# Kernel tuning notes

Hardware: AMD Instinct MI355X
Metric: run time of the kernel (lower is better)

Reference implementation:

```python
import jax, jax.numpy as jnp
import numpy as np

# regular 3x3 kernel grid: row0 = dy (i-1), row1 = dx (j-1), k = 3*i + j
RY = jnp.array([-1., -1., -1., 0., 0., 0., 1., 1., 1.], dtype=jnp.float32)
RX = jnp.array([-1., 0., 1., -1., 0., 1., -1., 0., 1.], dtype=jnp.float32)


def conv2d(x, w, b):
    # 3x3, stride 1, pad 1, NCHW/OIHW
    out = jax.lax.conv_general_dilated(
        x, w, window_strides=(1, 1), padding=((1, 1), (1, 1)),
        dimension_numbers=('NCHW', 'OIHW', 'NCHW'))
    return out + b[None, :, None, None]


def group_norm(x, gamma, beta, num_groups, eps=1e-5):
    N, C, H, W = x.shape
    xg = x.reshape(N, num_groups, C // num_groups, H, W)
    mu = xg.mean(axis=(2, 3, 4), keepdims=True)
    var = xg.var(axis=(2, 3, 4), keepdims=True)
    xn = ((xg - mu) * jax.lax.rsqrt(var + eps)).reshape(N, C, H, W)
    return xn * gamma[None, :, None, None] + beta[None, :, None, None]


def build_offset(tm, tr):
    # tm: [N,4,H,W] per-pixel 2x2 affine [[m00,m01],[m10,m11]]; tr: [N,2,H,W] (ty, tx)
    m00, m01, m10, m11 = tm[:, 0], tm[:, 1], tm[:, 2], tm[:, 3]  # [N,H,W]
    ry = RY[None, :, None, None]
    rx = RX[None, :, None, None]
    # offset = M @ R - R, plus translation broadcast to all 9 points
    dy = m00[:, None] * ry + m01[:, None] * rx - ry + tr[:, 0:1]  # [N,9,H,W]
    dx = m10[:, None] * ry + m11[:, None] * rx - rx + tr[:, 1:2]  # [N,9,H,W]
    return dy, dx


def bilinear_sample(img, py, px):
    # img: [N,C,H,W]; py, px: [N,K,H,W] sampling locations; zero padding outside
    N, C, H, W = img.shape
    K = py.shape[1]
    y0f = jnp.floor(py)
    x0f = jnp.floor(px)
    wy1 = py - y0f
    wx1 = px - x0f
    wy0 = 1.0 - wy1
    wx0 = 1.0 - wx1
    y0 = y0f.astype(jnp.int32)
    x0 = x0f.astype(jnp.int32)
    img_flat = img.reshape(N, C, H * W)

    def gather(yi, xi):
        valid = ((yi >= 0) & (yi < H) & (xi >= 0) & (xi < W)).astype(img.dtype)
        idx = jnp.clip(yi, 0, H - 1) * W + jnp.clip(xi, 0, W - 1)  # [N,K,H,W]
        flat = idx.reshape(N, 1, K * H * W)
        vals = jnp.take_along_axis(img_flat, jnp.broadcast_to(flat, (N, C, K * H * W)), axis=2)
        return vals.reshape(N, C, K, H, W) * valid[:, None]

    v00 = gather(y0, x0)
    v01 = gather(y0, x0 + 1)
    v10 = gather(y0 + 1, x0)
    v11 = gather(y0 + 1, x0 + 1)
    return (v00 * (wy0 * wx0)[:, None] + v01 * (wy0 * wx1)[:, None]
            + v10 * (wy1 * wx0)[:, None] + v11 * (wy1 * wx1)[:, None])


def deform_conv(x, dy, dx, w, pad=1, dil=1):
    # x: [N,Cin,H,W]; dy,dx: [N,9,H,W]; w: [Cout,Cin,3,3]; stride 1
    N, C, H, W = x.shape
    k = jnp.arange(9)
    ki = (k // 3).astype(x.dtype)[None, :, None, None]
    kj = (k % 3).astype(x.dtype)[None, :, None, None]
    hh = jnp.arange(H, dtype=x.dtype)[None, None, :, None]
    ww = jnp.arange(W, dtype=x.dtype)[None, None, None, :]
    py = hh - pad + dil * ki + dy  # [N,9,H,W]
    px = ww - pad + dil * kj + dx
    sampled = bilinear_sample(x, py, px)  # [N,C,9,H,W]
    return jnp.einsum('nckhw,ock->nohw', sampled, w.reshape(w.shape[0], C, 9))


def setup_inputs() -> dict:
    key = jax.random.key(0)
    ks = jax.random.split(key, 16)
    N, C, H, W = 4, 256, 64, 64
    x = jax.random.normal(ks[0], (N, C, H, W), jnp.float32)
    def p(k, shape, s):
        return jax.random.normal(k, shape, jnp.float32) * s
    s_off = 0.01                       # small STN heads -> modest offsets
    s_dc = 1.0 / np.sqrt(C * 9.0)      # deform-conv fan-in init
    return {
        'x': x,
        'w_tm1': p(ks[1], (4, C, 3, 3), s_off), 'b_tm1': jnp.zeros((4,), jnp.float32),
        'w_tr1': p(ks[2], (2, C, 3, 3), s_off), 'b_tr1': jnp.zeros((2,), jnp.float32),
        'w_dc1': p(ks[3], (C, C, 3, 3), s_dc),
        'g1': jnp.ones((C,), jnp.float32), 'be1': jnp.zeros((C,), jnp.float32),
        'w_tm2': p(ks[4], (4, C, 3, 3), s_off), 'b_tm2': jnp.zeros((4,), jnp.float32),
        'w_tr2': p(ks[5], (2, C, 3, 3), s_off), 'b_tr2': jnp.zeros((2,), jnp.float32),
        'w_dc2': p(ks[6], (C, C, 3, 3), s_dc),
        'g2': jnp.ones((C,), jnp.float32), 'be2': jnp.zeros((C,), jnp.float32),
    }


def reference(x, w_tm1, b_tm1, w_tr1, b_tr1, w_dc1, g1, be1,
              w_tm2, b_tm2, w_tr2, b_tr2, w_dc2, g2, be2):
    GROUPS = 32
    residual = x
    dy1, dx1 = build_offset(conv2d(x, w_tm1, b_tm1), conv2d(x, w_tr1, b_tr1))
    out = deform_conv(x, dy1, dx1, w_dc1)
    out = jax.nn.relu(group_norm(out, g1, be1, GROUPS))
    dy2, dx2 = build_offset(conv2d(out, w_tm2, b_tm2), conv2d(out, w_tr2, b_tr2))
    out = deform_conv(out, dy2, dx2, w_dc2)
    out = group_norm(out, g2, be2, GROUPS)
    return jax.nn.relu(out + residual)
```

## Files before the change

### kernel.cpp

```cpp
#include <hip/hip_runtime.h>


typedef unsigned int u32;
typedef unsigned short u16;
typedef __attribute__((ext_vector_type(8))) short bf16x8;
typedef __attribute__((ext_vector_type(4))) float floatx4;

#define HW 4096
#define CHW 1048576

static __device__ __forceinline__ float bf2f(u16 u) {
    union { u32 i; float f; } c; c.i = ((u32)u) << 16; return c.f;
}
static __device__ __forceinline__ u16 f2bf(float f) {
    union { float f; u32 i; } c; c.f = f;
    u32 x = c.i;
    return (u16)((x + 0x7FFFu + ((x >> 16) & 1u)) >> 16);
}
static __device__ __forceinline__ u32 cvtpk(float a, float b) {
    u32 r;
    asm("v_cvt_pk_bf16_f32 %0, %1, %2" : "=v"(r) : "v"(a), "v"(b));
    return r;
}
static __device__ __forceinline__ void lbar() {
    __builtin_amdgcn_sched_barrier(0);
    asm volatile("s_waitcnt lgkmcnt(0)" ::: "memory");
    __builtin_amdgcn_s_barrier();
    __builtin_amdgcn_sched_barrier(0);
}
static __device__ __forceinline__ float loadv(const void* p, long i, int f32) {
    return f32 ? ((const float*)p)[i] : bf2f(((const u16*)p)[i]);
}
static __device__ __forceinline__ int sniff_f32(const u32* __restrict__ xw) {
    int cnt = 0;
    #pragma unroll
    for (int s = 0; s < 16; ++s) {
        union { u32 i; float f; } c;
        c.i = xw[s * 131 + 7];
        float a = fabsf(c.f);
        if (a > 1e-8f && a < 1e4f) ++cnt;
    }
    return (cnt >= 8) ? 1 : 0;
}

__global__ __launch_bounds__(256) void k_prep_all(
    const void* __restrict__ x,
    const void* __restrict__ wdc1, const void* __restrict__ wdc2,
    const void* __restrict__ wtm1, const void* __restrict__ wtr1,
    const void* __restrict__ wtm2, const void* __restrict__ wtr2,
    u16* __restrict__ xT, u16* __restrict__ wTg1, u16* __restrict__ wTg2,
    u16* __restrict__ wT61, u16* __restrict__ wT62)
{
    __shared__ u16 T[32 * 258];
    const int f32 = sniff_f32((const u32*)x);
    const int b = blockIdx.x;
    const int tid = threadIdx.x;

    if (b < 512) {
        const int n = b >> 7, h = (b >> 1) & 63, half = b & 1;
        const int wbase = half << 5;
        const long sb = (long)n * CHW + (h << 6) + wbase;
        const int cb = tid >> 3;
        const int w0 = (tid & 7) << 2;
        if (f32) {
            const float* xp = (const float*)x;
            for (int it = 0; it < 8; ++it) {
                int c = (it << 5) + cb;
                float4 a = *(const float4*)(xp + sb + (long)c * HW + w0);
                T[(w0 + 0) * 258 + c] = f2bf(a.x);
                T[(w0 + 1) * 258 + c] = f2bf(a.y);
                T[(w0 + 2) * 258 + c] = f2bf(a.z);
                T[(w0 + 3) * 258 + c] = f2bf(a.w);
            }
        } else {
            const u16* xp = (const u16*)x;
            for (int it = 0; it < 8; ++it) {
                int c = (it << 5) + cb;
                uint2 v = *(const uint2*)(xp + sb + (long)c * HW + w0);
                T[(w0 + 0) * 258 + c] = (u16)(v.x & 0xFFFFu);
                T[(w0 + 1) * 258 + c] = (u16)(v.x >> 16);
                T[(w0 + 2) * 258 + c] = (u16)(v.y & 0xFFFFu);
                T[(w0 + 3) * 258 + c] = (u16)(v.y >> 16);
            }
        }
        __syncthreads();
        const int w = tid >> 3, cq = tid & 7;
        const u32* Tr = (const u32*)T;
        u16* ob = xT + (long)n * CHW + (long)((h << 6) + wbase + w) * 256 + cq * 32;
        #pragma unroll
        for (int s = 0; s < 4; ++s) {
            uint4 o;
            o.x = Tr[129 * w + 16 * cq + 4 * s + 0];
            o.y = Tr[129 * w + 16 * cq + 4 * s + 1];
            o.z = Tr[129 * w + 16 * cq + 4 * s + 2];
            o.w = Tr[129 * w + 16 * cq + 4 * s + 3];
            *(uint4*)&ob[s * 8] = o;
        }
    } else if (b < 2816) {
        const int r2 = (b >= 1664);
        const void* wdc = r2 ? wdc2 : wdc1;
        u16* wTg = r2 ? wTg2 : wTg1;
        int idx2 = (b - (r2 ? 1664 : 512)) * 256 + tid;
        int cp = idx2 & 15;
        int o  = (idx2 >> 4) & 255;
        int q  = idx2 >> 12;
        int k  = q >> 3;
        int c0 = ((q & 7) << 5) + (cp << 1);
        long s0 = (long)o * 2304 + c0 * 9 + k;
        ((u32*)wTg)[idx2] = cvtpk(loadv(wdc, s0, f32), loadv(wdc, s0 + 9, f32));
    } else {
        const int r2 = (b >= 2960);
        const void* wtm = r2 ? wtm2 : wtm1;
        const void* wtr = r2 ? wtr2 : wtr1;
        u16* wT6 = r2 ? wT62 : wT61;
        int i = (b - (r2 ? 2960 : 2816)) * 256 + tid;
        int q  = i >> 9;
        int o  = (i >> 5) & 15;
        int cc = i & 31;
        int k  = q >> 3;
        int c  = ((q & 7) << 5) + cc;
        float v = 0.f;
        if (o < 4)      v = loadv(wtm, (long)o * 2304 + c * 9 + k, f32);
        else if (o < 6) v = loadv(wtr, (long)(o - 4) * 2304 + c * 9 + k, f32);
        wT6[i] = f2bf(v);
    }
}

__global__ __launch_bounds__(1024, 4) void k_deform(
    const u16* __restrict__ srcT, const u16* __restrict__ wTg,
    const u16* __restrict__ wT6,
    const void* __restrict__ b_tm, const void* __restrict__ b_tr,
    const u32* __restrict__ xw,
    u16* __restrict__ raw, float* __restrict__ pstats, const int nhwc)
{
    __shared__ __align__(16) char shm[65536];
    __shared__ float tl[6 * 64];
    __shared__ int   g_y0[576];
    __shared__ int   g_x0[576];
    __shared__ float g_wy[576];
    __shared__ float g_wx[576];

    const int tid = threadIdx.x;
    const int bid = blockIdx.x;
    const int n = bid >> 6, h = bid & 63;
    const int lane = tid & 63;
    const int quad = lane >> 4;
    const int l16  = lane & 15;
    const int wv   = tid >> 6;
    const long nbase = (long)n * CHW;
    const u16* sp = srcT + nbase;

    {
        float (*red)[64][17] = (float (*)[64][17])shm;
        if (wv < 8) {
            floatx4 acc6[4];
            #pragma unroll
            for (int j = 0; j < 4; ++j) acc6[j] = (floatx4){0.f, 0.f, 0.f, 0.f};
            for (int qi = 0; qi < 9; ++qi) {
                const int q = wv * 9 + qi;
                const int k = q >> 3, cb = q & 7;
                const int ky = k / 3, kx = k % 3;
                const int row = h + ky - 1;
                const bool rv = (row >= 0) && (row < 64);
                bf16x8 av = *(const bf16x8*)&wT6[(((q << 4) + l16) << 5) + (quad << 3)];
                #pragma unroll
                for (int j = 0; j < 4; ++j) {
                    int psrc = (j << 4) + l16 + kx - 1;
                    bf16x8 bv = {0, 0, 0, 0, 0, 0, 0, 0};
                    if (rv && psrc >= 0 && psrc < 64)
                        bv = *(const bf16x8*)&sp[(((long)(row << 6) + psrc) << 8) + (cb << 5) + (quad << 3)];
                    acc6[j] = __builtin_amdgcn_mfma_f32_16x16x32_bf16(av, bv, acc6[j], 0, 0, 0);
                }
            }
            #pragma unroll
            for (int j = 0; j < 4; ++j)
                #pragma unroll
                for (int r = 0; r < 4; ++r)
                    red[wv][(j << 4) + l16][(quad << 2) + r] = acc6[j][r];
        }
        __syncthreads();
        if (tid < 384) {
            const int o = tid >> 6, px = tid & 63;
            float s = 0.f;
            #pragma unroll
            for (int v = 0; v < 8; ++v) s += red[v][px][o];
            const int f32 = sniff_f32(xw);
            float bias = (o < 4) ? loadv(b_tm, o, f32) : loadv(b_tr, o - 4, f32);
            tl[o * 64 + px] = s + bias;
        }
        __syncthreads();
    }

    if (tid < 576) {
        int i = tid;
        int k = i >> 6, ww2 = i & 63;
        float m00 = tl[ww2],        m01 = tl[64 + ww2];
        float m10 = tl[128 + ww2],  m11 = tl[192 + ww2];
        float tr0 = tl[256 + ww2],  tr1 = tl[320 + ww2];
        float ry = (float)(k / 3) - 1.f;
        float rx = (float)(k % 3) - 1.f;
        float dy = m00 * ry + m01 * rx - ry + tr0;
        float dx = m10 * ry + m11 * rx - rx + tr1;
        float py = (float)h + ry + dy;
        float px = (float)ww2 + rx + dx;
        float y0f = floorf(py), x0f = floorf(px);
        g_y0[i] = (int)y0f; g_x0[i] = (int)x0f;
        g_wy[i] = py - y0f; g_wx[i] = px - x0f;
    }
    __syncthreads();

    const int px   = tid >> 4;
    const int slot = tid & 15;
    const int kh   = wv >> 3;
    const int o0   = (wv & 7) << 5;
    const u32 xw_s = (u32)((px  & 7) << 2);
    const u32 xsw  = (u32)((l16 & 7) << 2);
    const u32 q4x  = (u32)(quad << 2);
    const u32 kh64 = (u32)(kh << 6);

    u32* Sl = (u32*)shm;

    floatx4 acc[2][4];
    #pragma unroll
    for (int a = 0; a < 2; ++a)
        #pragma unroll
        for (int g = 0; g < 4; ++g) acc[a][g] = (floatx4){0.f, 0.f, 0.f, 0.f};

    const int wlane = ((o0 + l16) << 5) + (quad << 3);
    const u16* wk = wTg + (kh << 15);

    u32 o00, o01, o10, o11;
    float cw00, cw01, cw10, cw11;
    const char* spb = (const char*)sp + (slot << 4);

    auto mkptr = [&](int k) {
        int gi = (k << 6) + px;
        int y0 = g_y0[gi], x0 = g_x0[gi];
        int yc0 = min(max(y0, 0), 63),     yc1 = min(max(y0 + 1, 0), 63);
        int xc0 = min(max(x0, 0), 63),     xc1 = min(max(x0 + 1, 0), 63);
        o00 = (u32)(((yc0 << 6) + xc0) << 9);
        o01 = (u32)(((yc0 << 6) + xc1) << 9);
        o10 = (u32)(((yc1 << 6) + xc0) << 9);
        o11 = (u32)(((yc1 << 6) + xc1) << 9);
    };
    auto mkcw = [&](int k) {
        int gi = (k << 6) + px;
        int y0 = g_y0[gi], x0 = g_x0[gi];
        float wy1 = g_wy[gi], wx1 = g_wx[gi];
        float wy0 = 1.f - wy1, wx0 = 1.f - wx1;
        bool yv0 = (y0 >= 0) && (y0 < 64);
        bool yv1 = (y0 >= -1) && (y0 < 63);
        bool xv0 = (x0 >= 0) && (x0 < 64);
        bool xv1 = (x0 >= -1) && (x0 < 63);
        cw00 = (yv0 && xv0) ? wy0 * wx0 : 0.f;
        cw01 = (yv0 && xv1) ? wy0 * wx1 : 0.f;
        cw10 = (yv1 && xv0) ? wy1 * wx0 : 0.f;
        cw11 = (yv1 && xv1) ? wy1 * wx1 : 0.f;
    };

    uint4 GA, GB, GC, GD, HA, HB, HC, HD;
    auto GATHER = [&]() {
        GA = *(const uint4*)(spb + o00);  HA = *(const uint4*)(spb + o00 + 256);
        GB = *(const uint4*)(spb + o01);  HB = *(const uint4*)(spb + o01 + 256);
        GC = *(const uint4*)(spb + o10);  HC = *(const uint4*)(spb + o10 + 256);
        GD = *(const uint4*)(spb + o11);  HD = *(const uint4*)(spb + o11 + 256);
    };

    bf16x8 W0[4], W1[4];

#define BIL(a, b, c, d) cvtpk( \
    fmaf(cw00, bf2f((u16)(a)), fmaf(cw01, bf2f((u16)(b)), \
    fmaf(cw10, bf2f((u16)(c)), cw11 * bf2f((u16)(d))))), \
    fmaf(cw00, bf2f((u16)((a) >> 16)), fmaf(cw01, bf2f((u16)((b) >> 16)), \
    fmaf(cw10, bf2f((u16)((c) >> 16)), cw11 * bf2f((u16)((d) >> 16))))))

    mkptr(0); GATHER();
    W0[0] = *(const bf16x8*)(wk + wlane);
    W1[0] = *(const bf16x8*)(wk + wlane + 512);
    W0[1] = *(const bf16x8*)(wk + 8192 + wlane);
    W1[1] = *(const bf16x8*)(wk + 8192 + wlane + 512);

    for (int k = 0; k < 9; ++k) {
        const int buf = k & 1;
        mkcw(k);
        uint4 v0 = make_uint4(BIL(GA.x, GB.x, GC.x, GD.x), BIL(GA.y, GB.y, GC.y, GD.y),
                              BIL(GA.z, GB.z, GC.z, GD.z), BIL(GA.w, GB.w, GC.w, GD.w));
        uint4 v1 = make_uint4(BIL(HA.x, HB.x, HC.x, HD.x), BIL(HA.y, HB.y, HC.y, HD.y),
                              BIL(HA.z, HB.z, HC.z, HD.z), BIL(HA.w, HB.w, HC.w, HD.w));
        u32* wp = &Sl[((u32)(buf << 13)) + ((u32)(px << 7)) + (((u32)(slot << 2)) ^ xw_s)];
        *(uint4*)wp = v0;
        *(uint4*)(wp + 64) = v1;
        if (k < 8) { mkptr(k + 1); GATHER(); }
        lbar();
        const u32* sb = &Sl[(u32)(buf << 13)];
        #pragma unroll
        for (int c = 0; c < 4; ++c) {
            const u32 offc = (((kh64 + (u32)(c << 4))) | q4x) ^ xsw;
            bf16x8 b0 = *(const bf16x8*)(sb + ((u32)(( 0 + l16) << 7)) + offc);
            bf16x8 b1 = *(const bf16x8*)(sb + ((u32)((16 + l16) << 7)) + offc);
            bf16x8 b2 = *(const bf16x8*)(sb + ((u32)((32 + l16) << 7)) + offc);
            bf16x8 b3 = *(const bf16x8*)(sb + ((u32)((48 + l16) << 7)) + offc);
            if (k < 8 || c < 2) {
                const int tc = c + 2;
                const u16* wb = wk + ((tc & 3) + ((tc >> 2) << 3)) * 8192;
                W0[tc & 3] = *(const bf16x8*)(wb + wlane);
                W1[tc & 3] = *(const bf16x8*)(wb + wlane + 512);
            }
            acc[0][0] = __builtin_amdgcn_mfma_f32_16x16x32_bf16(W0[c], b0, acc[0][0], 0, 0, 0);
            acc[0][1] = __builtin_amdgcn_mfma_f32_16x16x32_bf16(W0[c], b1, acc[0][1], 0, 0, 0);
            acc[0][2] = __builtin_amdgcn_mfma_f32_16x16x32_bf16(W0[c], b2, acc[0][2], 0, 0, 0);
            acc[0][3] = __builtin_amdgcn_mfma_f32_16x16x32_bf16(W0[c], b3, acc[0][3], 0, 0, 0);
            acc[1][0] = __builtin_amdgcn_mfma_f32_16x16x32_bf16(W1[c], b0, acc[1][0], 0, 0, 0);
            acc[1][1] = __builtin_amdgcn_mfma_f32_16x16x32_bf16(W1[c], b1, acc[1][1], 0, 0, 0);
            acc[1][2] = __builtin_amdgcn_mfma_f32_16x16x32_bf16(W1[c], b2, acc[1][2], 0, 0, 0);
            acc[1][3] = __builtin_amdgcn_mfma_f32_16x16x32_bf16(W1[c], b3, acc[1][3], 0, 0, 0);
        }
        wk += 65536;
    }
#undef BIL

    __syncthreads();
    {
        float* ms = (float*)shm;
        if (kh == 1) {
            #pragma unroll
            for (int a = 0; a < 2; ++a)
                #pragma unroll
                for (int g = 0; g < 4; ++g)
                    *(floatx4*)&ms[((((wv & 7) << 3) + (a << 2) + g) << 8) + (lane << 2)] = acc[a][g];
        }
        __syncthreads();
        if (kh == 0) {
            #pragma unroll
            for (int a = 0; a < 2; ++a)
                #pragma unroll
                for (int g = 0; g < 4; ++g) {
                    floatx4 t = *(const floatx4*)&ms[((((wv & 7) << 3) + (a << 2) + g) << 8) + (lane << 2)];
                    acc[a][g] += t;
                }
        }
    }

    if (kh == 0) {
        #pragma unroll
        for (int a = 0; a < 2; ++a) {
            float s1 = 0.f, s2 = 0.f;
            #pragma unroll
            for (int g = 0; g < 4; ++g)
                #pragma unroll
                for (int r = 0; r < 4; ++r) {
                    float v = acc[a][g][r];
                    s1 += v; s2 += v * v;
                }
            #pragma unroll
            for (int off = 1; off <= 16; off <<= 1) {
                s1 += __shfl_xor(s1, off, 64);
                s2 += __shfl_xor(s2, off, 64);
            }
            if ((lane & 31) == 0) {
                int gg = (o0 >> 3) + (a << 1) + (lane >> 5);
                pstats[((long)bid << 6) + (gg << 1)]     = s1;
                pstats[((long)bid << 6) + (gg << 1) + 1] = s2;
            }
        }

        if (nhwc) {
            u16* rb = raw + nbase + ((long)h << 14);
            #pragma unroll
            for (int a = 0; a < 2; ++a)
                #pragma unroll
                for (int g = 0; g < 4; ++g) {
                    int pxe = (g << 4) + l16;
                    int o = o0 + (a << 4) + (quad << 2);
                    u32 lo = cvtpk(acc[a][g][0], acc[a][g][1]);
                    u32 hi = cvtpk(acc[a][g][2], acc[a][g][3]);
                    *(uint2*)&rb[(pxe << 8) + o] = make_uint2(lo, hi);
                }
        } else {
            #pragma unroll
            for (int a = 0; a < 2; ++a)
                #pragma unroll
                for (int g = 0; g < 4; ++g)
                    #pragma unroll
                    for (int r = 0; r < 4; ++r) {
                        int o = o0 + (a << 4) + (quad << 2) + r;
                        raw[nbase + ((long)o << 12) + (h << 6) + (g << 4) + l16]
                            = f2bf(acc[a][g][r]);
                    }
        }
    }
}

__global__ __launch_bounds__(256) void k_gn_relu(
    const u16* __restrict__ raw, const float* __restrict__ pstats,
    const void* __restrict__ gamma, const void* __restrict__ beta,
    const u32* __restrict__ xw,
    u16* __restrict__ out1)
{
    __shared__ float sred[4][64];
    __shared__ float sl[64];
    const int f32 = sniff_f32(xw);
    const int tid = threadIdx.x;
    const int bid = blockIdx.x;
    const int n = bid >> 9;

    {
        const int v = tid & 63, part = tid >> 6;
        float a = 0.f;
        for (int j = part * 16; j < part * 16 + 16; ++j)
            a += pstats[(((long)n * 64 + j) << 6) + v];
        sred[part][v] = a;
        __syncthreads();
        if (tid < 64) sl[tid] = sred[0][tid] + sred[1][tid] + sred[2][tid] + sred[3][tid];
        __syncthreads();
    }

    const long i = (((long)bid) << 8) + tid;
    const int c0 = (int)((i << 3) & 255);
    const int g = c0 >> 3;
    float mean = sl[g * 2] * (1.f / 32768.f);
    float var  = sl[g * 2 + 1] * (1.f / 32768.f) - mean * mean;
    float rstd = rsqrtf(var + 1e-5f);

    float ga[8], be[8];
    if (f32) {
        float4 a0 = ((const float4*)gamma)[c0 >> 2];
        float4 a1 = ((const float4*)gamma)[(c0 >> 2) + 1];
        float4 b0 = ((const float4*)beta)[c0 >> 2];
        float4 b1 = ((const float4*)beta)[(c0 >> 2) + 1];
        ga[0]=a0.x; ga[1]=a0.y; ga[2]=a0.z; ga[3]=a0.w;
        ga[4]=a1.x; ga[5]=a1.y; ga[6]=a1.z; ga[7]=a1.w;
        be[0]=b0.x; be[1]=b0.y; be[2]=b0.z; be[3]=b0.w;
        be[4]=b1.x; be[5]=b1.y; be[6]=b1.z; be[7]=b1.w;
    } else {
        uint4 av = ((const uint4*)gamma)[c0 >> 3];
        uint4 bv = ((const uint4*)beta)[c0 >> 3];
        u32 aw[4] = {av.x, av.y, av.z, av.w};
        u32 bw[4] = {bv.x, bv.y, bv.z, bv.w};
        #pragma unroll
        for (int q = 0; q < 4; ++q) {
            ga[2*q] = bf2f((u16)(aw[q] & 0xFFFFu)); ga[2*q+1] = bf2f((u16)(aw[q] >> 16));
            be[2*q] = bf2f((u16)(bw[q] & 0xFFFFu)); be[2*q+1] = bf2f((u16)(bw[q] >> 16));
        }
    }

    uint4 p = ((const uint4*)raw)[i];
    u32 ww[4] = {p.x, p.y, p.z, p.w};
    u32 o[4];
    #pragma unroll
    for (int q = 0; q < 4; ++q) {
        float g0 = ga[2*q] * rstd,     g1 = ga[2*q+1] * rstd;
        float b0 = be[2*q] - mean*g0,  b1 = be[2*q+1] - mean*g1;
        float a = fmaxf(fmaf(bf2f((u16)(ww[q] & 0xFFFFu)), g0, b0), 0.f);
        float b = fmaxf(fmaf(bf2f((u16)(ww[q] >> 16)),     g1, b1), 0.f);
        o[q] = cvtpk(a, b);
    }
    ((uint4*)out1)[i] = make_uint4(o[0], o[1], o[2], o[3]);
}

__global__ __launch_bounds__(256) void k_gn_final(
    const u16* __restrict__ raw, const float* __restrict__ pstats,
    const void* __restrict__ gamma, const void* __restrict__ beta,
    const void* __restrict__ x,
    void* __restrict__ outp)
{
    __shared__ float rr[256];
    const int f32 = sniff_f32((const u32*)x);
    const int tid = threadIdx.x;
    const long e0 = ((long)blockIdx.x) << 11;
    const int n = (int)(e0 >> 20);
    const int c0 = (int)((e0 >> 12) & 255);
    const int g = c0 >> 3;

    {
        int j = tid & 127, sv = tid >> 7;
        rr[tid] = (j < 64) ? pstats[(((long)n * 64 + j) << 6) + (g << 1) + sv] : 0.f;
        __syncthreads();
        #pragma unroll
        for (int s = 64; s >= 1; s >>= 1) {
            if ((tid & 127) < s) rr[tid] += rr[tid + s];
            __syncthreads();
        }
    }
    float mean = rr[0] * (1.f / 32768.f);
    float var  = rr[128] * (1.f / 32768.f) - mean * mean;
    float rstd = rsqrtf(var + 1e-5f);

    const long i = blockIdx.x * 256 + tid;
    const long e = i << 3;
    const int c = (int)((e >> 12) & 255);
    float ga = loadv(gamma, c, f32) * rstd;
    float be = loadv(beta, c, f32) - mean * ga;
    uint4 p = ((const uint4*)raw)[i];
    u32 ww[4] = {p.x, p.y, p.z, p.w};
    float v[8];
    #pragma unroll
    for (int q = 0; q < 4; ++q) {
        v[2 * q + 0] = fmaxf(fmaf(bf2f((u16)(ww[q] & 0xFFFFu)), ga, be) + loadv(x, e + 2 * q + 0, f32), 0.f);
        v[2 * q + 1] = fmaxf(fmaf(bf2f((u16)(ww[q] >> 16)),     ga, be) + loadv(x, e + 2 * q + 1, f32), 0.f);
    }
    if (f32) {
        float4* op = (float4*)((float*)outp + e);
        op[0] = make_float4(v[0], v[1], v[2], v[3]);
        op[1] = make_float4(v[4], v[5], v[6], v[7]);
    } else {
        uint4 o;
        o.x = cvtpk(v[0], v[1]);
        o.y = cvtpk(v[2], v[3]);
        o.z = cvtpk(v[4], v[5]);
        o.w = cvtpk(v[6], v[7]);
        ((uint4*)outp)[i] = o;
    }
}

extern "C" void kernel_launch(void* const* d_in, const int* in_sizes, int n_in,
                              void* d_out, int out_size, void* d_ws, size_t ws_size,
                              hipStream_t stream) {
    const void* x     = d_in[0];
    const void* w_tm1 = d_in[1];
    const void* b_tm1 = d_in[2];
    const void* w_tr1 = d_in[3];
    const void* b_tr1 = d_in[4];
    const void* w_dc1 = d_in[5];
    const void* g1    = d_in[6];
    const void* be1   = d_in[7];
    const void* w_tm2 = d_in[8];
    const void* b_tm2 = d_in[9];
    const void* w_tr2 = d_in[10];
    const void* b_tr2 = d_in[11];
    const void* w_dc2 = d_in[12];
    const void* g2    = d_in[13];
    const void* be2   = d_in[14];

    char* wsb = (char*)d_ws;
    u16*   xT     = (u16*)wsb;
    u16*   raw    = (u16*)(wsb + 8388608);
    u16*   wTg1   = (u16*)(wsb + 16777216);
    u16*   wTg2   = (u16*)(wsb + 17956864);
    u16*   wT61   = (u16*)(wsb + 19136512);
    u16*   wT62   = (u16*)(wsb + 19210240);
    float* pstats = (float*)(wsb + 19283968);
    u16*   out1   = xT;
    const u32* xw = (const u32*)x;

    k_prep_all<<<3104, 256, 0, stream>>>(x, w_dc1, w_dc2, w_tm1, w_tr1, w_tm2, w_tr2,
                                         xT, wTg1, wTg2, wT61, wT62);
    k_deform  <<<256, 1024, 0, stream>>>(xT, wTg1, wT61, b_tm1, b_tr1, xw, raw, pstats, 1);
    k_gn_relu <<<2048, 256, 0, stream>>>(raw, pstats, g1, be1, xw, out1);
    k_deform  <<<256, 1024, 0, stream>>>(out1, wTg2, wT62, b_tm2, b_tr2, xw, raw, pstats, 0);
    k_gn_final<<<2048, 256, 0, stream>>>(raw, pstats, g2, be2, x, d_out);
}
```

Baseline: 211.6 us.

## Fuse group-norm epilogues into deform kernels via cooperative grid sync

The deform conv kernel becomes a cooperative kernel. After writing per-block partial statistics it does a grid-wide sync, reduces the group statistics in shared memory, and applies GroupNorm+ReLU (or GroupNorm+residual+ReLU) straight from the accumulator registers. This removes the bf16 raw intermediate round trip through global memory and two separate elementwise kernel launches. In exchange, all blocks must be co-resident and wait at a grid barrier, and the final-mode stores stay scalar and strided per channel.

```diff
diff --git a/kernel.cpp b/kernel.cpp
--- a/kernel.cpp
+++ b/kernel.cpp
@@ -1,4 +1,7 @@
 #include <hip/hip_runtime.h>
+#include <hip/hip_cooperative_groups.h>
+
+namespace cg = cooperative_groups;
 
 
 typedef unsigned int u32;
@@ -126,12 +129,16 @@
     }
 }
 
-__global__ __launch_bounds__(1024, 4) void k_deform(
+__global__ __launch_bounds__(1024, 4) void k_deform_fused(
     const u16* __restrict__ srcT, const u16* __restrict__ wTg,
     const u16* __restrict__ wT6,
     const void* __restrict__ b_tm, const void* __restrict__ b_tr,
     const u32* __restrict__ xw,
-    u16* __restrict__ raw, float* __restrict__ pstats, const int nhwc)
+    float* __restrict__ pstats,
+    const void* __restrict__ gamma, const void* __restrict__ beta,
+    const void* __restrict__ xres,
+    void* __restrict__ outp,
+    const int final_mode)
 {
     __shared__ __align__(16) char shm[65536];
     __shared__ float tl[6 * 64];
@@ -363,153 +370,72 @@
                 pstats[((long)bid << 6) + (gg << 1) + 1] = s2;
             }
         }
-
-        if (nhwc) {
-            u16* rb = raw + nbase + ((long)h << 14);
-            #pragma unroll
-            for (int a = 0; a < 2; ++a)
-                #pragma unroll
-                for (int g = 0; g < 4; ++g) {
-                    int pxe = (g << 4) + l16;
-                    int o = o0 + (a << 4) + (quad << 2);
-                    u32 lo = cvtpk(acc[a][g][0], acc[a][g][1]);
-                    u32 hi = cvtpk(acc[a][g][2], acc[a][g][3]);
-                    *(uint2*)&rb[(pxe << 8) + o] = make_uint2(lo, hi);
-                }
-        } else {
-            #pragma unroll
-            for (int a = 0; a < 2; ++a)
-                #pragma unroll
-                for (int g = 0; g < 4; ++g)
-                    #pragma unroll
-                    for (int r = 0; r < 4; ++r) {
-                        int o = o0 + (a << 4) + (quad << 2) + r;
-                        raw[nbase + ((long)o << 12) + (h << 6) + (g << 4) + l16]
-                            = f2bf(acc[a][g][r]);
-                    }
-        }
-    }
-}
-
-__global__ __launch_bounds__(256) void k_gn_relu(
-    const u16* __restrict__ raw, const float* __restrict__ pstats,
-    const void* __restrict__ gamma, const void* __restrict__ beta,
-    const u32* __restrict__ xw,
-    u16* __restrict__ out1)
-{
-    __shared__ float sred[4][64];
-    __shared__ float sl[64];
-    const int f32 = sniff_f32(xw);
-    const int tid = threadIdx.x;
-    const int bid = blockIdx.x;
-    const int n = bid >> 9;
+    }
+
+    __threadfence();
+    cg::this_grid().sync();
 
     {
+        float* sred = (float*)shm;
         const int v = tid & 63, part = tid >> 6;
         float a = 0.f;
-        for (int j = part * 16; j < part * 16 + 16; ++j)
+        #pragma unroll
+        for (int j = part * 4; j < part * 4 + 4; ++j)
             a += pstats[(((long)n * 64 + j) << 6) + v];
-        sred[part][v] = a;
-        __syncthreads();
-        if (tid < 64) sl[tid] = sred[0][tid] + sred[1][tid] + sred[2][tid] + sred[3][tid];
-        __syncthreads();
-    }
-
-    const long i = (((long)bid) << 8) + tid;
-    const int c0 = (int)((i << 3) & 255);
-    const int g = c0 >> 3;
-    float mean = sl[g * 2] * (1.f / 32768.f);
-    float var  = sl[g * 2 + 1] * (1.f / 32768.f) - mean * mean;
-    float rstd = rsqrtf(var + 1e-5f);
-
-    float ga[8], be[8];
-    if (f32) {
-        float4 a0 = ((const float4*)gamma)[c0 >> 2];
-        float4 a1 = ((const float4*)gamma)[(c0 >> 2) + 1];
-        float4 b0 = ((const float4*)beta)[c0 >> 2];
-        float4 b1 = ((const float4*)beta)[(c0 >> 2) + 1];
-        ga[0]=a0.x; ga[1]=a0.y; ga[2]=a0.z; ga[3]=a0.w;
-        ga[4]=a1.x; ga[5]=a1.y; ga[6]=a1.z; ga[7]=a1.w;
-        be[0]=b0.x; be[1]=b0.y; be[2]=b0.z; be[3]=b0.w;
-        be[4]=b1.x; be[5]=b1.y; be[6]=b1.z; be[7]=b1.w;
-    } else {
-        uint4 av = ((const uint4*)gamma)[c0 >> 3];
-        uint4 bv = ((const uint4*)beta)[c0 >> 3];
-        u32 aw[4] = {av.x, av.y, av.z, av.w};
-        u32 bw[4] = {bv.x, bv.y, bv.z, bv.w};
-        #pragma unroll
-        for (int q = 0; q < 4; ++q) {
-            ga[2*q] = bf2f((u16)(aw[q] & 0xFFFFu)); ga[2*q+1] = bf2f((u16)(aw[q] >> 16));
-            be[2*q] = bf2f((u16)(bw[q] & 0xFFFFu)); be[2*q+1] = bf2f((u16)(bw[q] >> 16));
-        }
-    }
-
-    uint4 p = ((const uint4*)raw)[i];
-    u32 ww[4] = {p.x, p.y, p.z, p.w};
-    u32 o[4];
-    #pragma unroll
-    for (int q = 0; q < 4; ++q) {
-        float g0 = ga[2*q] * rstd,     g1 = ga[2*q+1] * rstd;
-        float b0 = be[2*q] - mean*g0,  b1 = be[2*q+1] - mean*g1;
-        float a = fmaxf(fmaf(bf2f((u16)(ww[q] & 0xFFFFu)), g0, b0), 0.f);
-        float b = fmaxf(fmaf(bf2f((u16)(ww[q] >> 16)),     g1, b1), 0.f);
-        o[q] = cvtpk(a, b);
-    }
-    ((uint4*)out1)[i] = make_uint4(o[0], o[1], o[2], o[3]);
-}
-
-__global__ __launch_bounds__(256) void k_gn_final(
-    const u16* __restrict__ raw, const float* __restrict__ pstats,
-    const void* __restrict__ gamma, const void* __restrict__ beta,
-    const void* __restrict__ x,
-    void* __restrict__ outp)
-{
-    __shared__ float rr[256];
-    const int f32 = sniff_f32((const u32*)x);
-    const int tid = threadIdx.x;
-    const long e0 = ((long)blockIdx.x) << 11;
-    const int n = (int)(e0 >> 20);
-    const int c0 = (int)((e0 >> 12) & 255);
-    const int g = c0 >> 3;
-
-    {
-        int j = tid & 127, sv = tid >> 7;
-        rr[tid] = (j < 64) ? pstats[(((long)n * 64 + j) << 6) + (g << 1) + sv] : 0.f;
-        __syncthreads();
-        #pragma unroll
-        for (int s = 64; s >= 1; s >>= 1) {
-            if ((tid & 127) < s) rr[tid] += rr[tid + s];
-            __syncthreads();
-        }
-    }
-    float mean = rr[0] * (1.f / 32768.f);
-    float var  = rr[128] * (1.f / 32768.f) - mean * mean;
-    float rstd = rsqrtf(var + 1e-5f);
-
-    const long i = blockIdx.x * 256 + tid;
-    const long e = i << 3;
-    const int c = (int)((e >> 12) & 255);
-    float ga = loadv(gamma, c, f32) * rstd;
-    float be = loadv(beta, c, f32) - mean * ga;
-    uint4 p = ((const uint4*)raw)[i];
-    u32 ww[4] = {p.x, p.y, p.z, p.w};
-    float v[8];
-    #pragma unroll
-    for (int q = 0; q < 4; ++q) {
-        v[2 * q + 0] = fmaxf(fmaf(bf2f((u16)(ww[q] & 0xFFFFu)), ga, be) + loadv(x, e + 2 * q + 0, f32), 0.f);
-        v[2 * q + 1] = fmaxf(fmaf(bf2f((u16)(ww[q] >> 16)),     ga, be) + loadv(x, e + 2 * q + 1, f32), 0.f);
-    }
-    if (f32) {
-        float4* op = (float4*)((float*)outp + e);
-        op[0] = make_float4(v[0], v[1], v[2], v[3]);
-        op[1] = make_float4(v[4], v[5], v[6], v[7]);
-    } else {
-        uint4 o;
-        o.x = cvtpk(v[0], v[1]);
-        o.y = cvtpk(v[2], v[3]);
-        o.z = cvtpk(v[4], v[5]);
-        o.w = cvtpk(v[6], v[7]);
-        ((uint4*)outp)[i] = o;
+        sred[part * 64 + v] = a;
+        __syncthreads();
+        if (tid < 64) {
+            float s = 0.f;
+            #pragma unroll
+            for (int p = 0; p < 16; ++p) s += sred[p * 64 + tid];
+            tl[tid] = s;
+        }
+        __syncthreads();
+    }
+
+    if (kh == 0) {
+        const int f32 = sniff_f32(xw);
+        #pragma unroll
+        for (int a2 = 0; a2 < 2; ++a2) {
+            const int ob = o0 + (a2 << 4) + (quad << 2);
+            const int g = ob >> 3;
+            float mean = tl[g * 2] * (1.f / 32768.f);
+            float var  = tl[g * 2 + 1] * (1.f / 32768.f) - mean * mean;
+            float rstd = rsqrtf(var + 1e-5f);
+            float ga[4], be[4];
+            #pragma unroll
+            for (int r = 0; r < 4; ++r) {
+                ga[r] = loadv(gamma, ob + r, f32) * rstd;
+                be[r] = loadv(beta,  ob + r, f32) - mean * ga[r];
+            }
+            if (final_mode == 0) {
+                u16* rb = (u16*)outp + nbase + ((long)h << 14);
+                #pragma unroll
+                for (int g2 = 0; g2 < 4; ++g2) {
+                    int pxe = (g2 << 4) + l16;
+                    float v0 = fmaxf(fmaf(acc[a2][g2][0], ga[0], be[0]), 0.f);
+                    float v1 = fmaxf(fmaf(acc[a2][g2][1], ga[1], be[1]), 0.f);
+                    float v2 = fmaxf(fmaf(acc[a2][g2][2], ga[2], be[2]), 0.f);
+                    float v3 = fmaxf(fmaf(acc[a2][g2][3], ga[3], be[3]), 0.f);
+                    *(uint2*)&rb[((long)pxe << 8) + ob] =
+                        make_uint2(cvtpk(v0, v1), cvtpk(v2, v3));
+                }
+            } else {
+                #pragma unroll
+                for (int r = 0; r < 4; ++r) {
+                    const long base = nbase + ((long)(ob + r) << 12) + (h << 6);
+                    #pragma unroll
+                    for (int g2 = 0; g2 < 4; ++g2) {
+                        int pxe = (g2 << 4) + l16;
+                        float v = fmaf(acc[a2][g2][r], ga[r], be[r])
+                                + loadv(xres, base + pxe, f32);
+                        v = fmaxf(v, 0.f);
+                        if (f32) ((float*)outp)[base + pxe] = v;
+                        else     ((u16*)outp)[base + pxe] = f2bf(v);
+                    }
+                }
+            }
+        }
     }
 }
 
@@ -534,7 +460,6 @@
 
     char* wsb = (char*)d_ws;
     u16*   xT     = (u16*)wsb;
-    u16*   raw    = (u16*)(wsb + 8388608);
     u16*   wTg1   = (u16*)(wsb + 16777216);
     u16*   wTg2   = (u16*)(wsb + 17956864);
     u16*   wT61   = (u16*)(wsb + 19136512);
@@ -545,8 +470,27 @@
 
     k_prep_all<<<3104, 256, 0, stream>>>(x, w_dc1, w_dc2, w_tm1, w_tr1, w_tm2, w_tr2,
                                          xT, wTg1, wTg2, wT61, wT62);
-    k_deform  <<<256, 1024, 0, stream>>>(xT, wTg1, wT61, b_tm1, b_tr1, xw, raw, pstats, 1);
-    k_gn_relu <<<2048, 256, 0, stream>>>(raw, pstats, g1, be1, xw, out1);
-    k_deform  <<<256, 1024, 0, stream>>>(out1, wTg2, wT62, b_tm2, b_tr2, xw, raw, pstats, 0);
-    k_gn_final<<<2048, 256, 0, stream>>>(raw, pstats, g2, be2, x, d_out);
-}
+
+    {
+        const u16* srcT = xT;  const u16* wTg = wTg1;  const u16* wT6 = wT61;
+        const void* btm = b_tm1; const void* btr = b_tr1;
+        const u32* xwv = xw; float* pst = pstats;
+        const void* gam = g1; const void* bet = be1;
+        const void* xr = nullptr; void* op = (void*)out1; int fm = 0;
+        void* args[] = {&srcT, &wTg, &wT6, &btm, &btr, &xwv, &pst,
+                        &gam, &bet, &xr, &op, &fm};
+        hipLaunchCooperativeKernel((const void*)k_deform_fused,
+                                   dim3(256), dim3(1024), args, 0, stream);
+    }
+    {
+        const u16* srcT = out1; const u16* wTg = wTg2; const u16* wT6 = wT62;
+        const void* btm = b_tm2; const void* btr = b_tr2;
+        const u32* xwv = xw; float* pst = pstats;
+        const void* gam = g2; const void* bet = be2;
+        const void* xr = x; void* op = d_out; int fm = 1;
+        void* args[] = {&srcT, &wTg, &wT6, &btm, &btr, &xwv, &pst,
+                        &gam, &bet, &xr, &op, &fm};
+        hipLaunchCooperativeKernel((const void*)k_deform_fused,
+                                   dim3(256), dim3(1024), args, 0, stream);
+    }
+}
```

Result: slower. 435.7 us (+105.9%).
